# Kernel tuning notes

Hardware: AMD Instinct MI355X
Metric: run time of the kernel (lower is better)

## Reference

```python
import jax, jax.numpy as jnp
import numpy as np

VOCAB, SEQ, HID, HEADS, LAYERS = 30522, 512, 768, 12, 12
DH = HID // HEADS
BATCH = 32
LN_EPS = 1e-12


def setup_inputs() -> dict:
    key = jax.random.key(0)
    ks = jax.random.split(key, 12)
    x = jax.random.randint(ks[0], (BATCH, SEQ), 0, VOCAB)
    word_emb = jax.random.normal(ks[1], (VOCAB, HID), jnp.float32) * 0.02
    pos_emb = jax.random.normal(ks[2], (SEQ, HID), jnp.float32) * 0.02
    type_emb = jax.random.normal(ks[3], (HID,), jnp.float32) * 0.02
    ln_g = jnp.ones((HID,), jnp.float32)
    ln_b = jnp.zeros((HID,), jnp.float32)
    # per-layer mats (original uses torch.ones placeholders; random here for a
    # meaningful correctness baseline, same math)
    W = jax.random.normal(ks[4], (LAYERS, HID, HID), jnp.float32) * 0.02
    b = jax.random.normal(ks[5], (LAYERS, HID), jnp.float32) * 0.02
    M = jax.random.normal(ks[6], (LAYERS, HEADS, SEQ, SEQ), jnp.float32) * (1.0 / np.sqrt(SEQ))
    last_w = jax.random.normal(ks[7], (HID, HID), jnp.float32) * 0.02
    last_b = jax.random.normal(ks[8], (HID,), jnp.float32) * 0.02
    return {"x": x, "word_emb": word_emb, "pos_emb": pos_emb, "type_emb": type_emb,
            "ln_g": ln_g, "ln_b": ln_b, "W": W, "b": b, "M": M,
            "last_w": last_w, "last_b": last_b}


def _layernorm(h, g, beta):
    mu = jnp.mean(h, axis=-1, keepdims=True)
    var = jnp.mean(jnp.square(h - mu), axis=-1, keepdims=True)
    return (h - mu) * jax.lax.rsqrt(var + LN_EPS) * g + beta


def _multihead_mut(h, Mi):
    # original: per (batch, head) loop of (dh, msl) @ (msl, msl).
    # out[b,t,h,d] = sum_s h[b,s,h,d] * M[h,s,t]
    b, s, _ = h.shape
    hx = h.reshape(b, s, HEADS, DH)
    out = jnp.einsum('bshd,hst->bthd', hx, Mi)
    return out.reshape(b, s, HID)


def reference(x, word_emb, pos_emb, type_emb, ln_g, ln_b, W, b, M, last_w, last_b):
    # BertEmbeddings: word + position + token_type(all zeros -> single row) + LayerNorm
    h = word_emb[x] + pos_emb[None, :, :] + type_emb
    h = _layernorm(h, ln_g, ln_b)
    for i in range(LAYERS):
        h = h @ W[i].T                 # [B,S,D]
        h = _multihead_mut(h, M[i])    # per-head seq mixing
        h = jax.nn.relu(h + b[i])
    return h @ last_w.T + last_b
```

## Files before the change

kernel.cpp:

```cpp
#include <hip/hip_runtime.h>
#include <hip/hip_bf16.h>

#define SEQ 512
#define HID 768
#define HEADS 12
#define DH 64
#define LAYERS 12
#define BATCH 32
#define TOK (BATCH*SEQ)

typedef __hip_bfloat16 hbf16;
typedef __attribute__((ext_vector_type(8))) __bf16 bf16x8;
typedef __attribute__((ext_vector_type(4))) __bf16 bf16x4;
typedef __attribute__((ext_vector_type(4))) float f32x4;

__global__ __launch_bounds__(256) void embed_ln_k(
    const int* __restrict__ x, const float* __restrict__ we,
    const float* __restrict__ pe, const float* __restrict__ te,
    const float* __restrict__ g, const float* __restrict__ be,
    __bf16* __restrict__ h) {
  const int tok = blockIdx.x;
  const int s = tok & (SEQ - 1);
  const int wid = x[tok];
  const int tid = threadIdx.x;
  float v[3];
  float sum = 0.f, sq = 0.f;
#pragma unroll
  for (int j = 0; j < 3; j++) {
    int c = tid + j * 256;
    float val = we[(size_t)wid * HID + c] + pe[(size_t)s * HID + c] + te[c];
    v[j] = val; sum += val; sq += val * val;
  }
#pragma unroll
  for (int off = 32; off > 0; off >>= 1) {
    sum += __shfl_down(sum, off);
    sq  += __shfl_down(sq, off);
  }
  __shared__ float rs_[4], rq_[4];
  const int wv = tid >> 6;
  if ((tid & 63) == 0) { rs_[wv] = sum; rq_[wv] = sq; }
  __syncthreads();
  sum = rs_[0] + rs_[1] + rs_[2] + rs_[3];
  sq  = rq_[0] + rq_[1] + rq_[2] + rq_[3];
  const float mu  = sum * (1.f / HID);
  const float var = sq * (1.f / HID) - mu * mu;
  const float inv = rsqrtf(var + 1e-12f);
#pragma unroll
  for (int j = 0; j < 3; j++) {
    int c = tid + j * 256;
    float o = (v[j] - mu) * inv * g[c] + be[c];
    h[(size_t)tok * HID + c] = (__bf16)o;
  }
}

__global__ __launch_bounds__(256) void transpose_m_k(
    const float* __restrict__ Ml, __bf16* __restrict__ Mt) {
  __shared__ float tile[64][68];
  const int head = blockIdx.z;
  const int t0 = blockIdx.x * 64, s0 = blockIdx.y * 64;
  const float* src = Ml + (size_t)head * SEQ * SEQ;
  __bf16* dst = Mt + (size_t)head * SEQ * SEQ;
  const int tid = threadIdx.x;
#pragma unroll
  for (int it = 0; it < 4; it++) {
    int e = (it * 256 + tid) * 4;
    int r = e >> 6, c = e & 63;
    *(f32x4*)&tile[r][c] = *(const f32x4*)&src[(size_t)(s0 + r) * SEQ + t0 + c];
  }
  __syncthreads();
#pragma unroll
  for (int it = 0; it < 2; it++) {
    int e = (it * 256 + tid) * 8;
    int r = e >> 6, c = e & 63;
    bf16x8 vv;
#pragma unroll
    for (int j = 0; j < 8; j++) vv[j] = (__bf16)tile[c + j][r];
    *(bf16x8*)&dst[(size_t)(t0 + r) * SEQ + s0 + c] = vv;
  }
}

__global__ __launch_bounds__(256) void dense_t_k(
    const float* __restrict__ Wl, const __bf16* __restrict__ hin,
    __bf16* __restrict__ h2t) {
  __shared__ __bf16 Al[128][40];
  __shared__ __bf16 Bl[128][40];
  const int n0 = blockIdx.x * 128;
  const int m0 = blockIdx.y * 128;
  const int tid = threadIdx.x;
  const int wave = tid >> 6, lane = tid & 63;
  const int wm = (wave >> 1) << 6, wn = (wave & 1) << 6;
  const int lm = lane & 15, q = lane >> 4;
  f32x4 acc[4][4];
#pragma unroll
  for (int i = 0; i < 4; i++)
#pragma unroll
    for (int j = 0; j < 4; j++) acc[i][j] = {0.f, 0.f, 0.f, 0.f};

  for (int k0 = 0; k0 < HID; k0 += 32) {
#pragma unroll
    for (int it = 0; it < 4; it++) {
      int e = (it * 256 + tid) * 4;
      int r = e >> 5, c = e & 31;
      f32x4 w4 = *(const f32x4*)&Wl[(size_t)(m0 + r) * HID + k0 + c];
      bf16x4 b4;
#pragma unroll
      for (int j = 0; j < 4; j++) b4[j] = (__bf16)w4[j];
      *(bf16x4*)&Al[r][c] = b4;
    }
#pragma unroll
    for (int it = 0; it < 2; it++) {
      int e = (it * 256 + tid) * 8;
      int r = e >> 5, c = e & 31;
      *(bf16x8*)&Bl[r][c] = *(const bf16x8*)&hin[(size_t)(n0 + r) * HID + k0 + c];
    }
    __syncthreads();
    bf16x8 af[4], bfr[4];
#pragma unroll
    for (int i = 0; i < 4; i++) {
      af[i]  = *(const bf16x8*)&Al[wm + i * 16 + lm][q * 8];
      bfr[i] = *(const bf16x8*)&Bl[wn + i * 16 + lm][q * 8];
    }
#pragma unroll
    for (int mi = 0; mi < 4; mi++)
#pragma unroll
      for (int ni = 0; ni < 4; ni++)
        acc[mi][ni] = __builtin_amdgcn_mfma_f32_16x16x32_bf16(af[mi], bfr[ni], acc[mi][ni], 0, 0, 0);
    __syncthreads();
  }
#pragma unroll
  for (int mi = 0; mi < 4; mi++)
#pragma unroll
    for (int ni = 0; ni < 4; ni++)
#pragma unroll
      for (int r = 0; r < 4; r++) {
        int dout = m0 + wm + mi * 16 + q * 4 + r;
        int n = n0 + wn + ni * 16 + lm;
        h2t[(size_t)dout * TOK + n] = (__bf16)acc[mi][ni][r];
      }
}

__global__ __launch_bounds__(256) void mix_relu_k(
    const __bf16* __restrict__ Mt, const __bf16* __restrict__ h2t,
    const float* __restrict__ bias_l, __bf16* __restrict__ hout) {
  __shared__ __bf16 Al[256][40];
  __shared__ __bf16 Bl[64][40];
  const int t0 = blockIdx.x * 256;
  const int head = blockIdx.y;
  const int b = blockIdx.z;
  const __bf16* Mh = Mt + (size_t)head * SEQ * SEQ;
  const __bf16* X  = h2t + (size_t)head * DH * TOK + (size_t)b * SEQ;
  const int tid = threadIdx.x;
  const int wave = tid >> 6, lane = tid & 63;
  const int wm = wave << 6;
  const int lm = lane & 15, q = lane >> 4;
  f32x4 acc[4][4];
#pragma unroll
  for (int i = 0; i < 4; i++)
#pragma unroll
    for (int j = 0; j < 4; j++) acc[i][j] = {0.f, 0.f, 0.f, 0.f};

  for (int s0 = 0; s0 < SEQ; s0 += 32) {
#pragma unroll
    for (int it = 0; it < 4; it++) {
      int e = (it * 256 + tid) * 8;
      int r = e >> 5, c = e & 31;
      *(bf16x8*)&Al[r][c] = *(const bf16x8*)&Mh[(size_t)(t0 + r) * SEQ + s0 + c];
    }
    {
      int e = tid * 8;
      int r = e >> 5, c = e & 31;
      *(bf16x8*)&Bl[r][c] = *(const bf16x8*)&X[(size_t)r * TOK + s0 + c];
    }
    __syncthreads();
    bf16x8 af[4], bfr[4];
#pragma unroll
    for (int i = 0; i < 4; i++) {
      af[i]  = *(const bf16x8*)&Al[wm + i * 16 + lm][q * 8];
      bfr[i] = *(const bf16x8*)&Bl[i * 16 + lm][q * 8];
    }
#pragma unroll
    for (int mi = 0; mi < 4; mi++)
#pragma unroll
      for (int ni = 0; ni < 4; ni++)
        acc[mi][ni] = __builtin_amdgcn_mfma_f32_16x16x32_bf16(af[mi], bfr[ni], acc[mi][ni], 0, 0, 0);
    __syncthreads();
  }
  float bias[4];
#pragma unroll
  for (int ni = 0; ni < 4; ni++) bias[ni] = bias_l[head * DH + ni * 16 + lm];
#pragma unroll
  for (int mi = 0; mi < 4; mi++)
#pragma unroll
    for (int ni = 0; ni < 4; ni++)
#pragma unroll
      for (int r = 0; r < 4; r++) {
        int t = t0 + wm + mi * 16 + q * 4 + r;
        float vv = fmaxf(acc[mi][ni][r] + bias[ni], 0.f);
        hout[((size_t)b * SEQ + t) * HID + head * DH + ni * 16 + lm] = (__bf16)vv;
      }
}

__global__ __launch_bounds__(256) void dense_nat_k(
    const __bf16* __restrict__ hin, const float* __restrict__ lw,
    const float* __restrict__ lb, float* __restrict__ out) {
  __shared__ __bf16 Al[128][40];
  __shared__ __bf16 Bl[128][40];
  const int m0 = blockIdx.x * 128;
  const int n0 = blockIdx.y * 128;
  const int tid = threadIdx.x;
  const int wave = tid >> 6, lane = tid & 63;
  const int wm = (wave >> 1) << 6, wn = (wave & 1) << 6;
  const int lm = lane & 15, q = lane >> 4;
  f32x4 acc[4][4];
#pragma unroll
  for (int i = 0; i < 4; i++)
#pragma unroll
    for (int j = 0; j < 4; j++) acc[i][j] = {0.f, 0.f, 0.f, 0.f};

  for (int k0 = 0; k0 < HID; k0 += 32) {
#pragma unroll
    for (int it = 0; it < 2; it++) {
      int e = (it * 256 + tid) * 8;
      int r = e >> 5, c = e & 31;
      *(bf16x8*)&Al[r][c] = *(const bf16x8*)&hin[(size_t)(m0 + r) * HID + k0 + c];
    }
#pragma unroll
    for (int it = 0; it < 4; it++) {
      int e = (it * 256 + tid) * 4;
      int r = e >> 5, c = e & 31;
      f32x4 w4 = *(const f32x4*)&lw[(size_t)(n0 + r) * HID + k0 + c];
      bf16x4 b4;
#pragma unroll
      for (int j = 0; j < 4; j++) b4[j] = (__bf16)w4[j];
      *(bf16x4*)&Bl[r][c] = b4;
    }
    __syncthreads();
    bf16x8 af[4], bfr[4];
#pragma unroll
    for (int i = 0; i < 4; i++) {
      af[i]  = *(const bf16x8*)&Al[wm + i * 16 + lm][q * 8];
      bfr[i] = *(const bf16x8*)&Bl[wn + i * 16 + lm][q * 8];
    }
#pragma unroll
    for (int mi = 0; mi < 4; mi++)
#pragma unroll
      for (int ni = 0; ni < 4; ni++)
        acc[mi][ni] = __builtin_amdgcn_mfma_f32_16x16x32_bf16(af[mi], bfr[ni], acc[mi][ni], 0, 0, 0);
    __syncthreads();
  }
#pragma unroll
  for (int mi = 0; mi < 4; mi++)
#pragma unroll
    for (int ni = 0; ni < 4; ni++) {
      float bias = lb[n0 + wn + ni * 16 + lm];
#pragma unroll
      for (int r = 0; r < 4; r++) {
        int tok = m0 + wm + mi * 16 + q * 4 + r;
        int n = n0 + wn + ni * 16 + lm;
        out[(size_t)tok * HID + n] = acc[mi][ni][r] + bias;
      }
    }
}

extern "C" void kernel_launch(void* const* d_in, const int* in_sizes, int n_in,
                              void* d_out, int out_size, void* d_ws, size_t ws_size,
                              hipStream_t stream) {
  const int*   x   = (const int*)d_in[0];
  const float* we  = (const float*)d_in[1];
  const float* pe  = (const float*)d_in[2];
  const float* te  = (const float*)d_in[3];
  const float* lng = (const float*)d_in[4];
  const float* lnb = (const float*)d_in[5];
  const float* W   = (const float*)d_in[6];
  const float* bb  = (const float*)d_in[7];
  const float* M   = (const float*)d_in[8];
  const float* lw  = (const float*)d_in[9];
  const float* lb  = (const float*)d_in[10];

  __bf16* Mt  = (__bf16*)d_ws;
  __bf16* hA  = Mt + (size_t)HEADS * SEQ * SEQ;
  __bf16* h2t = hA + (size_t)TOK * HID;
  float* out = (float*)d_out;

  embed_ln_k<<<TOK, 256, 0, stream>>>(x, we, pe, te, lng, lnb, hA);
  for (int l = 0; l < LAYERS; l++) {
    transpose_m_k<<<dim3(8, 8, HEADS), 256, 0, stream>>>(M + (size_t)l * HEADS * SEQ * SEQ, Mt);
    dense_t_k<<<dim3(TOK / 128, HID / 128), 256, 0, stream>>>(W + (size_t)l * HID * HID, hA, h2t);
    mix_relu_k<<<dim3(2, HEADS, BATCH), 256, 0, stream>>>(Mt, h2t, bb + (size_t)l * HID, hA);
  }
  dense_nat_k<<<dim3(TOK / 128, HID / 128), 256, 0, stream>>>(hA, lw, lb, out);
}
```

Before: 1.151 ms.

## Pre-convert weights to bf16 and load GEMM tiles via async global-to-LDS copies

Converts all layer weights and the final weight to bf16 once up front, and transposes all M matrices in a single batched launch instead of one launch per layer. The three GEMM kernels now stage tiles with global_load_lds 16-byte async copies into unpadded LDS, replacing register round-trips and in-loop fp32->bf16 conversion. This reduces per-iteration load work and the number of kernel launches. The cost is a larger workspace, and the LDS layout loses its padding, which may cause bank conflicts on the fragment reads.

```diff
diff --git a/kernel.cpp b/kernel.cpp
--- a/kernel.cpp
+++ b/kernel.cpp
@@ -9,10 +9,25 @@
 #define BATCH 32
 #define TOK (BATCH*SEQ)
 
-typedef __hip_bfloat16 hbf16;
 typedef __attribute__((ext_vector_type(8))) __bf16 bf16x8;
 typedef __attribute__((ext_vector_type(4))) __bf16 bf16x4;
 typedef __attribute__((ext_vector_type(4))) float f32x4;
+
+typedef __attribute__((address_space(1))) const void gvoid;
+typedef __attribute__((address_space(3))) void svoid;
+__device__ __forceinline__ void async_cp16(const void* g, void* l) {
+  __builtin_amdgcn_global_load_lds((gvoid*)g, (svoid*)l, 16, 0, 0);
+}
+
+__global__ __launch_bounds__(256) void convert_k(
+    const float* __restrict__ src, __bf16* __restrict__ dst) {
+  int i = (blockIdx.x * 256 + threadIdx.x) * 4;
+  f32x4 v = *(const f32x4*)&src[i];
+  bf16x4 b;
+#pragma unroll
+  for (int j = 0; j < 4; j++) b[j] = (__bf16)v[j];
+  *(bf16x4*)&dst[i] = b;
+}
 
 __global__ __launch_bounds__(256) void embed_ln_k(
     const int* __restrict__ x, const float* __restrict__ we,
@@ -53,13 +68,13 @@
   }
 }
 
-__global__ __launch_bounds__(256) void transpose_m_k(
-    const float* __restrict__ Ml, __bf16* __restrict__ Mt) {
+__global__ __launch_bounds__(256) void transpose_all_m_k(
+    const float* __restrict__ M, __bf16* __restrict__ Mt) {
   __shared__ float tile[64][68];
-  const int head = blockIdx.z;
+  const int lh = blockIdx.z;
   const int t0 = blockIdx.x * 64, s0 = blockIdx.y * 64;
-  const float* src = Ml + (size_t)head * SEQ * SEQ;
-  __bf16* dst = Mt + (size_t)head * SEQ * SEQ;
+  const float* src = M + (size_t)lh * SEQ * SEQ;
+  __bf16* dst = Mt + (size_t)lh * SEQ * SEQ;
   const int tid = threadIdx.x;
 #pragma unroll
   for (int it = 0; it < 4; it++) {
@@ -80,16 +95,17 @@
 }
 
 __global__ __launch_bounds__(256) void dense_t_k(
-    const float* __restrict__ Wl, const __bf16* __restrict__ hin,
+    const __bf16* __restrict__ Wb, const __bf16* __restrict__ hin,
     __bf16* __restrict__ h2t) {
-  __shared__ __bf16 Al[128][40];
-  __shared__ __bf16 Bl[128][40];
+  __shared__ __bf16 Al[128 * 32];
+  __shared__ __bf16 Bl[128 * 32];
   const int n0 = blockIdx.x * 128;
   const int m0 = blockIdx.y * 128;
   const int tid = threadIdx.x;
   const int wave = tid >> 6, lane = tid & 63;
   const int wm = (wave >> 1) << 6, wn = (wave & 1) << 6;
   const int lm = lane & 15, q = lane >> 4;
+  const int lrow = lane >> 2, lcol = (lane & 3) * 8;
   f32x4 acc[4][4];
 #pragma unroll
   for (int i = 0; i < 4; i++)
@@ -98,27 +114,18 @@
 
   for (int k0 = 0; k0 < HID; k0 += 32) {
 #pragma unroll
-    for (int it = 0; it < 4; it++) {
-      int e = (it * 256 + tid) * 4;
-      int r = e >> 5, c = e & 31;
-      f32x4 w4 = *(const f32x4*)&Wl[(size_t)(m0 + r) * HID + k0 + c];
-      bf16x4 b4;
-#pragma unroll
-      for (int j = 0; j < 4; j++) b4[j] = (__bf16)w4[j];
-      *(bf16x4*)&Al[r][c] = b4;
-    }
-#pragma unroll
     for (int it = 0; it < 2; it++) {
-      int e = (it * 256 + tid) * 8;
-      int r = e >> 5, c = e & 31;
-      *(bf16x8*)&Bl[r][c] = *(const bf16x8*)&hin[(size_t)(n0 + r) * HID + k0 + c];
+      int c = wave * 2 + it;
+      int row = c * 16 + lrow;
+      async_cp16(&Wb[(size_t)(m0 + row) * HID + k0 + lcol], &Al[c * 512 + lane * 8]);
+      async_cp16(&hin[(size_t)(n0 + row) * HID + k0 + lcol], &Bl[c * 512 + lane * 8]);
     }
     __syncthreads();
     bf16x8 af[4], bfr[4];
 #pragma unroll
     for (int i = 0; i < 4; i++) {
-      af[i]  = *(const bf16x8*)&Al[wm + i * 16 + lm][q * 8];
-      bfr[i] = *(const bf16x8*)&Bl[wn + i * 16 + lm][q * 8];
+      af[i]  = *(const bf16x8*)&Al[(wm + i * 16 + lm) * 32 + q * 8];
+      bfr[i] = *(const bf16x8*)&Bl[(wn + i * 16 + lm) * 32 + q * 8];
     }
 #pragma unroll
     for (int mi = 0; mi < 4; mi++)
@@ -140,19 +147,20 @@
 }
 
 __global__ __launch_bounds__(256) void mix_relu_k(
-    const __bf16* __restrict__ Mt, const __bf16* __restrict__ h2t,
+    const __bf16* __restrict__ Mtl, const __bf16* __restrict__ h2t,
     const float* __restrict__ bias_l, __bf16* __restrict__ hout) {
-  __shared__ __bf16 Al[256][40];
-  __shared__ __bf16 Bl[64][40];
+  __shared__ __bf16 Al[256 * 32];
+  __shared__ __bf16 Bl[64 * 32];
   const int t0 = blockIdx.x * 256;
   const int head = blockIdx.y;
   const int b = blockIdx.z;
-  const __bf16* Mh = Mt + (size_t)head * SEQ * SEQ;
+  const __bf16* Mh = Mtl + (size_t)head * SEQ * SEQ;
   const __bf16* X  = h2t + (size_t)head * DH * TOK + (size_t)b * SEQ;
   const int tid = threadIdx.x;
   const int wave = tid >> 6, lane = tid & 63;
   const int wm = wave << 6;
   const int lm = lane & 15, q = lane >> 4;
+  const int lrow = lane >> 2, lcol = (lane & 3) * 8;
   f32x4 acc[4][4];
 #pragma unroll
   for (int i = 0; i < 4; i++)
@@ -162,21 +170,20 @@
   for (int s0 = 0; s0 < SEQ; s0 += 32) {
 #pragma unroll
     for (int it = 0; it < 4; it++) {
-      int e = (it * 256 + tid) * 8;
-      int r = e >> 5, c = e & 31;
-      *(bf16x8*)&Al[r][c] = *(const bf16x8*)&Mh[(size_t)(t0 + r) * SEQ + s0 + c];
+      int c = wave * 4 + it;
+      int row = c * 16 + lrow;
+      async_cp16(&Mh[(size_t)(t0 + row) * SEQ + s0 + lcol], &Al[c * 512 + lane * 8]);
     }
     {
-      int e = tid * 8;
-      int r = e >> 5, c = e & 31;
-      *(bf16x8*)&Bl[r][c] = *(const bf16x8*)&X[(size_t)r * TOK + s0 + c];
+      int row = wave * 16 + lrow;
+      async_cp16(&X[(size_t)row * TOK + s0 + lcol], &Bl[wave * 512 + lane * 8]);
     }
     __syncthreads();
     bf16x8 af[4], bfr[4];
 #pragma unroll
     for (int i = 0; i < 4; i++) {
-      af[i]  = *(const bf16x8*)&Al[wm + i * 16 + lm][q * 8];
-      bfr[i] = *(const bf16x8*)&Bl[i * 16 + lm][q * 8];
+      af[i]  = *(const bf16x8*)&Al[(wm + i * 16 + lm) * 32 + q * 8];
+      bfr[i] = *(const bf16x8*)&Bl[(i * 16 + lm) * 32 + q * 8];
     }
 #pragma unroll
     for (int mi = 0; mi < 4; mi++)
@@ -201,16 +208,17 @@
 }
 
 __global__ __launch_bounds__(256) void dense_nat_k(
-    const __bf16* __restrict__ hin, const float* __restrict__ lw,
+    const __bf16* __restrict__ hin, const __bf16* __restrict__ lwb,
     const float* __restrict__ lb, float* __restrict__ out) {
-  __shared__ __bf16 Al[128][40];
-  __shared__ __bf16 Bl[128][40];
+  __shared__ __bf16 Al[128 * 32];
+  __shared__ __bf16 Bl[128 * 32];
   const int m0 = blockIdx.x * 128;
   const int n0 = blockIdx.y * 128;
   const int tid = threadIdx.x;
   const int wave = tid >> 6, lane = tid & 63;
   const int wm = (wave >> 1) << 6, wn = (wave & 1) << 6;
   const int lm = lane & 15, q = lane >> 4;
+  const int lrow = lane >> 2, lcol = (lane & 3) * 8;
   f32x4 acc[4][4];
 #pragma unroll
   for (int i = 0; i < 4; i++)
@@ -220,26 +228,17 @@
   for (int k0 = 0; k0 < HID; k0 += 32) {
 #pragma unroll
     for (int it = 0; it < 2; it++) {
-      int e = (it * 256 + tid) * 8;
-      int r = e >> 5, c = e & 31;
-      *(bf16x8*)&Al[r][c] = *(const bf16x8*)&hin[(size_t)(m0 + r) * HID + k0 + c];
-    }
-#pragma unroll
-    for (int it = 0; it < 4; it++) {
-      int e = (it * 256 + tid) * 4;
-      int r = e >> 5, c = e & 31;
-      f32x4 w4 = *(const f32x4*)&lw[(size_t)(n0 + r) * HID + k0 + c];
-      bf16x4 b4;
-#pragma unroll
-      for (int j = 0; j < 4; j++) b4[j] = (__bf16)w4[j];
-      *(bf16x4*)&Bl[r][c] = b4;
+      int c = wave * 2 + it;
+      int row = c * 16 + lrow;
+      async_cp16(&hin[(size_t)(m0 + row) * HID + k0 + lcol], &Al[c * 512 + lane * 8]);
+      async_cp16(&lwb[(size_t)(n0 + row) * HID + k0 + lcol], &Bl[c * 512 + lane * 8]);
     }
     __syncthreads();
     bf16x8 af[4], bfr[4];
 #pragma unroll
     for (int i = 0; i < 4; i++) {
-      af[i]  = *(const bf16x8*)&Al[wm + i * 16 + lm][q * 8];
-      bfr[i] = *(const bf16x8*)&Bl[wn + i * 16 + lm][q * 8];
+      af[i]  = *(const bf16x8*)&Al[(wm + i * 16 + lm) * 32 + q * 8];
+      bfr[i] = *(const bf16x8*)&Bl[(wn + i * 16 + lm) * 32 + q * 8];
     }
 #pragma unroll
     for (int mi = 0; mi < 4; mi++)
@@ -278,15 +277,20 @@
   const float* lb  = (const float*)d_in[10];
 
   __bf16* Mt  = (__bf16*)d_ws;
-  __bf16* hA  = Mt + (size_t)HEADS * SEQ * SEQ;
+  __bf16* Wb  = Mt + (size_t)LAYERS * HEADS * SEQ * SEQ;
+  __bf16* lwb = Wb + (size_t)LAYERS * HID * HID;
+  __bf16* hA  = lwb + (size_t)HID * HID;
   __bf16* h2t = hA + (size_t)TOK * HID;
   float* out = (float*)d_out;
 
+  convert_k<<<LAYERS * HID * HID / 1024, 256, 0, stream>>>(W, Wb);
+  convert_k<<<HID * HID / 1024, 256, 0, stream>>>(lw, lwb);
+  transpose_all_m_k<<<dim3(8, 8, LAYERS * HEADS), 256, 0, stream>>>(M, Mt);
   embed_ln_k<<<TOK, 256, 0, stream>>>(x, we, pe, te, lng, lnb, hA);
   for (int l = 0; l < LAYERS; l++) {
-    transpose_m_k<<<dim3(8, 8, HEADS), 256, 0, stream>>>(M + (size_t)l * HEADS * SEQ * SEQ, Mt);
-    dense_t_k<<<dim3(TOK / 128, HID / 128), 256, 0, stream>>>(W + (size_t)l * HID * HID, hA, h2t);
-    mix_relu_k<<<dim3(2, HEADS, BATCH), 256, 0, stream>>>(Mt, h2t, bb + (size_t)l * HID, hA);
-  }
-  dense_nat_k<<<dim3(TOK / 128, HID / 128), 256, 0, stream>>>(hA, lw, lb, out);
-}
+    dense_t_k<<<dim3(TOK / 128, HID / 128), 256, 0, stream>>>(Wb + (size_t)l * HID * HID, hA, h2t);
+    mix_relu_k<<<dim3(2, HEADS, BATCH), 256, 0, stream>>>(Mt + (size_t)l * HEADS * SEQ * SEQ, h2t,
+                                                          bb + (size_t)l * HID, hA);
+  }
+  dense_nat_k<<<dim3(TOK / 128, HID / 128), 256, 0, stream>>>(hA, lwb, lb, out);
+}
```

After: 1.018 ms. -11.6%, faster.
